# Kernel optimization log

Hardware: AMD Instinct MI355X
Metric: run time of the kernel (lower is better)

Reference implementation:

```python
import jax, jax.numpy as jnp
import numpy as np

N_NODES = 100000
N_EDGES = 3200000
NUM_GRAPHS = 64
NEG_SLOPE = 0.2  # PyG GATConv default leaky_relu slope


def gat_conv(x, src, dst, W, att_src, att_dst, bias, heads, out_ch, concat):
    """PyG GATConv (default args: add_self_loops=True, negative_slope=0.2).
    src/dst already include self loops."""
    n = x.shape[0]
    h = (x @ W).reshape(n, heads, out_ch)              # [N,H,C]
    a_src = jnp.sum(h * att_src, axis=-1)              # [N,H]
    a_dst = jnp.sum(h * att_dst, axis=-1)              # [N,H]
    e = jax.nn.leaky_relu(a_src[src] + a_dst[dst], NEG_SLOPE)  # [E,H]
    # segment softmax over destination nodes
    m = jax.ops.segment_max(e, dst, num_segments=n)
    ex = jnp.exp(e - m[dst])
    denom = jax.ops.segment_sum(ex, dst, num_segments=n)
    alpha = ex / (denom[dst] + 1e-16)                  # [E,H]
    msg = h[src] * alpha[:, :, None]                   # [E,H,C]
    out = jax.ops.segment_sum(msg, dst, num_segments=n)  # [N,H,C]
    if concat:
        out = out.reshape(n, heads * out_ch)
    else:
        out = out.mean(axis=1)
    return out + bias


def setup_inputs() -> dict:
    key = jax.random.key(0)
    ks = jax.random.split(key, 12)
    x = jax.random.normal(ks[0], (N_NODES, 4), dtype=jnp.float32)
    edge_index = jax.random.randint(ks[1], (2, N_EDGES), 0, N_NODES, dtype=jnp.int64)
    batch = jnp.sort(jax.random.randint(ks[2], (N_NODES,), 0, NUM_GRAPHS, dtype=jnp.int64))
    s = 0.1
    return {
        "x": x,
        "edge_index": edge_index,
        "batch": batch,
        "W1": jax.random.normal(ks[3], (4, 64), dtype=jnp.float32) * s,
        "att_src1": jax.random.normal(ks[4], (2, 32), dtype=jnp.float32) * s,
        "att_dst1": jax.random.normal(ks[5], (2, 32), dtype=jnp.float32) * s,
        "bias1": jnp.zeros((64,), dtype=jnp.float32),
        "W2": jax.random.normal(ks[6], (64, 64), dtype=jnp.float32) * s,
        "att_src2": jax.random.normal(ks[7], (1, 64), dtype=jnp.float32) * s,
        "att_dst2": jax.random.normal(ks[8], (1, 64), dtype=jnp.float32) * s,
        "bias2": jnp.zeros((64,), dtype=jnp.float32),
    }


def reference(x, edge_index, batch, W1, att_src1, att_dst1, bias1, W2, att_src2, att_dst2, bias2):
    n = x.shape[0]
    loops = jnp.arange(n, dtype=edge_index.dtype)
    src = jnp.concatenate([edge_index[0], loops])
    dst = jnp.concatenate([edge_index[1], loops])
    h = gat_conv(x, src, dst, W1, att_src1, att_dst1, bias1, heads=2, out_ch=32, concat=True)
    h = jax.nn.elu(h)
    # dropout is identity in eval mode
    h = gat_conv(h, src, dst, W2, att_src2, att_dst2, bias2, heads=1, out_ch=64, concat=False)
    # global_mean_pool
    sums = jax.ops.segment_sum(h, batch, num_segments=NUM_GRAPHS)
    counts = jax.ops.segment_sum(jnp.ones((n,), h.dtype), batch, num_segments=NUM_GRAPHS)
    return sums / jnp.maximum(counts, 1.0)[:, None]
```

## Files before the change

### kernel.cpp

```cpp
#include <hip/hip_runtime.h>
#include <hip/hip_bf16.h>
#include <hip/hip_fp16.h>
#include <math.h>


__device__ __forceinline__ float leaky(float x) { return x >= 0.f ? x : 0.2f * x; }
__device__ __forceinline__ int iclamp(int v, int lo, int hi) {
  return v < lo ? lo : (v > hi ? hi : v);
}
__device__ __forceinline__ unsigned char f8(float v) {
  return (unsigned char)(__builtin_amdgcn_cvt_pk_fp8_f32(v, v, 0, false) & 0xff);
}

typedef __attribute__((ext_vector_type(8))) _Float16 f16x8;
typedef __attribute__((ext_vector_type(4))) float f32x4;
typedef __attribute__((ext_vector_type(2))) float f32x2;

#define NBUCK 1024
#define BSHIFT 7
#define BCAP 4608
#define CSRSZ (NBUCK * BCAP)
#define MAXR 16

__global__ __launch_bounds__(256) void k_att1(
    const float* __restrict__ x, const float* __restrict__ W1,
    const float* __restrict__ att_src1, const float* __restrict__ att_dst1,
    float* __restrict__ a_src1, float* __restrict__ a_dst1, int n) {
  __shared__ float W1s[256];
  int t = threadIdx.x;
  W1s[t] = W1[t];
  __syncthreads();
  int node = blockIdx.x * 4 + (t >> 6);
  int lane = t & 63;
  if (node >= n) return;
  float4 xr = ((const float4*)x)[node];
  float h = xr.x * W1s[lane] + xr.y * W1s[64 + lane] + xr.z * W1s[128 + lane] + xr.w * W1s[192 + lane];
  float vs = h * att_src1[lane];
  float vd = h * att_dst1[lane];
  #pragma unroll
  for (int m = 16; m >= 1; m >>= 1) { vs += __shfl_xor(vs, m); vd += __shfl_xor(vd, m); }
  if ((lane & 31) == 0) {
    int head = lane >> 5;
    a_src1[node * 2 + head] = vs;
    a_dst1[node * 2 + head] = vd;
  }
}

__global__ __launch_bounds__(1024) void k_bscatter(
    const int* __restrict__ ei, int E, int n, int* __restrict__ bcur,
    unsigned* __restrict__ pairs) {
  __shared__ int h[NBUCK];
  __shared__ int cur[NBUCK];
  int t = threadIdx.x;
  if (t < NBUCK) h[t] = 0;
  __syncthreads();
  int chunk = (E + gridDim.x - 1) / gridDim.x;
  int beg = blockIdx.x * chunk;
  int end = beg + chunk; if (end > E) end = E;
  unsigned pR[MAXR];
  unsigned short bR[MAXR];
  int cntr = 0;
  for (int i = beg + t; i < end && cntr < MAXR; i += 1024) {
    int s = iclamp(ei[i], 0, n - 1);
    int d = iclamp(ei[E + i], 0, n - 1);
    int bkt = d >> BSHIFT;
    pR[cntr] = ((unsigned)(d & 127) << 25) | (unsigned)s;
    bR[cntr] = (unsigned short)bkt;
    atomicAdd(&h[bkt], 1);
    ++cntr;
  }
  __syncthreads();
  if (t < NBUCK) cur[t] = t * BCAP + (h[t] ? atomicAdd(&bcur[t], h[t]) : 0);
  __syncthreads();
  for (int k = 0; k < cntr; ++k) {
    int bkt = bR[k];
    int pos = atomicAdd(&cur[bkt], 1);
    if (pos >= bkt * BCAP && pos < (bkt + 1) * BCAP) pairs[pos] = pR[k];
  }
}

__global__ __launch_bounds__(256) void k_bbuild(
    const unsigned* __restrict__ pairs, const int* __restrict__ bcur,
    int n, int* __restrict__ rowbeg, int* __restrict__ rowend,
    int* __restrict__ csr) {
  int b = blockIdx.x;
  int node0 = b << BSHIFT;
  if (node0 >= n) return;
  int base = b * BCAP;
  int cnt = iclamp(bcur[b], 0, BCAP);
  __shared__ int sh[128];
  __shared__ int cur[128];
  int t = threadIdx.x;
  if (t < 128) sh[t] = 0;
  __syncthreads();
  for (int i = t; i < cnt; i += 256)
    atomicAdd(&sh[pairs[base + i] >> 25], 1);
  __syncthreads();
  int v = (t < 128) ? sh[t] : 0;
  for (int ofs = 1; ofs < 128; ofs <<= 1) {
    int u = (t >= ofs && t < 128) ? sh[t - ofs] : 0;
    __syncthreads();
    if (t < 128) sh[t] += u;
    __syncthreads();
  }
  if (t < 128) {
    int off = sh[t] - v;
    cur[t] = off;
    int node = node0 + t;
    if (node < n) {
      rowbeg[node] = base + off;
      rowend[node] = base + off + v;
    }
  }
  __syncthreads();
  for (int i = t; i < cnt; i += 256) {
    unsigned p = pairs[base + i];
    int l = p >> 25;
    int r = atomicAdd(&cur[l], 1);
    int pos = base + r;
    if (pos >= 0 && pos < CSRSZ) csr[pos] = (int)(p & 0x1ffffffu);
  }
}

__global__ __launch_bounds__(256) void k_gat1(
    const float* __restrict__ x, const float* __restrict__ W1,
    const float* __restrict__ a_src1, const float* __restrict__ a_dst1,
    const int* __restrict__ rowbeg, const int* __restrict__ rowend,
    const int* __restrict__ csr,
    const float* __restrict__ bias1, __half* __restrict__ hB,
    int n) {
  __shared__ float W1s[256];
  int t = threadIdx.x;
  W1s[t] = W1[t];
  __syncthreads();
  int lane = t & 63;
  int nd = lane >> 4, sub = lane & 15;
  int node = (blockIdx.x * 4 + (t >> 6)) * 4 + nd;
  bool valid = node < n;
  int nc = valid ? node : 0;
  int beg = valid ? iclamp(rowbeg[nc], 0, CSRSZ) : 0;
  int end = valid ? iclamp(rowend[nc], beg, CSRSZ) : 0;
  float2 ad = ((const float2*)a_dst1)[nc];
  const float4* xp = (const float4*)x;
  const float2* asp = (const float2*)a_src1;
  float A0 = 0.f, A1 = 0.f, A2 = 0.f, A3 = 0.f, dn0 = 0.f;
  float B0 = 0.f, B1 = 0.f, B2 = 0.f, B3 = 0.f, dn1 = 0.f;
  for (int e = beg + sub; e < end; e += 16) {
    int s = iclamp(csr[e], 0, n - 1);
    float2 as = asp[s];
    float ex0 = __expf(leaky(as.x + ad.x));
    float ex1 = __expf(leaky(as.y + ad.y));
    float4 xr = xp[s];
    dn0 += ex0; dn1 += ex1;
    A0 = fmaf(ex0, xr.x, A0); A1 = fmaf(ex0, xr.y, A1);
    A2 = fmaf(ex0, xr.z, A2); A3 = fmaf(ex0, xr.w, A3);
    B0 = fmaf(ex1, xr.x, B0); B1 = fmaf(ex1, xr.y, B1);
    B2 = fmaf(ex1, xr.z, B2); B3 = fmaf(ex1, xr.w, B3);
  }
  bool lo = (sub < 8);
  float C0, C1, C2, C3, dnC, sA, sB;
  sA = __shfl_xor(A0, 8); sB = __shfl_xor(B0, 8); C0 = lo ? A0 + sA : B0 + sB;
  sA = __shfl_xor(A1, 8); sB = __shfl_xor(B1, 8); C1 = lo ? A1 + sA : B1 + sB;
  sA = __shfl_xor(A2, 8); sB = __shfl_xor(B2, 8); C2 = lo ? A2 + sA : B2 + sB;
  sA = __shfl_xor(A3, 8); sB = __shfl_xor(B3, 8); C3 = lo ? A3 + sA : B3 + sB;
  sA = __shfl_xor(dn0, 8); sB = __shfl_xor(dn1, 8); dnC = lo ? dn0 + sA : dn1 + sB;
  #pragma unroll
  for (int m = 4; m >= 1; m >>= 1) {
    C0 += __shfl_xor(C0, m); C1 += __shfl_xor(C1, m);
    C2 += __shfl_xor(C2, m); C3 += __shfl_xor(C3, m);
    dnC += __shfl_xor(dnC, m);
  }
  float2 asn = asp[nc];
  float4 xs = xp[nc];
  float exs = __expf(leaky((lo ? asn.x : asn.y) + (lo ? ad.x : ad.y)));
  dnC += exs;
  C0 = fmaf(exs, xs.x, C0); C1 = fmaf(exs, xs.y, C1);
  C2 = fmaf(exs, xs.z, C2); C3 = fmaf(exs, xs.w, C3);
  float inv = 1.0f / (dnC + 1e-16f);
  if (valid) {
    int f0 = sub * 4;
    float vv[4];
    #pragma unroll
    for (int i = 0; i < 4; ++i) {
      int f = f0 + i;
      float accv = C0 * W1s[f] + C1 * W1s[64 + f] + C2 * W1s[128 + f] + C3 * W1s[192 + f];
      float v = accv * inv + bias1[f];
      vv[i] = v > 0.f ? v : expm1f(v);
    }
    __half2 h01 = __float22half2_rn(make_float2(vv[0], vv[1]));
    __half2 h23 = __float22half2_rn(make_float2(vv[2], vv[3]));
    uint2 pk;
    pk.x = *(unsigned*)&h01;
    pk.y = *(unsigned*)&h23;
    *(uint2*)(hB + (size_t)node * 64 + f0) = pk;
  }
}

__global__ __launch_bounds__(256) void k_lin2(
    const __half* __restrict__ hB, const float* __restrict__ W2,
    const float* __restrict__ att_src2, const float* __restrict__ att_dst2,
    float* __restrict__ a_src2, float* __restrict__ a_dst2,
    unsigned char* __restrict__ hC, int n) {
  __shared__ __attribute__((aligned(16))) _Float16 Whi[64 * 72];
  __shared__ __attribute__((aligned(16))) _Float16 Wlo[64 * 72];
  int t = threadIdx.x;
  for (int i = t; i < 4096; i += 256) {
    int k = i >> 6, col = i & 63;
    float w = W2[i];
    _Float16 hi = (_Float16)w;
    _Float16 lo = (_Float16)(w - (float)hi);
    Whi[col * 72 + k] = hi;
    Wlo[col * 72 + k] = lo;
  }
  __syncthreads();
  int wave = t >> 6, lane = t & 63;
  int quad = lane >> 4, c = lane & 15;
  int m0 = blockIdx.x * 64 + wave * 16;
  if (m0 >= n) return;
  int mrow = m0 + c; if (mrow > n - 1) mrow = n - 1;
  const _Float16* hrow = (const _Float16*)(hB + (size_t)mrow * 64);
  f16x8 a0 = *(const f16x8*)(hrow + quad * 8);
  f16x8 a1 = *(const f16x8*)(hrow + 32 + quad * 8);
  f32x4 zero = {0.f, 0.f, 0.f, 0.f};
  f32x4 acc[4] = {zero, zero, zero, zero};
  #pragma unroll
  for (int tt = 0; tt < 4; ++tt) {
    int nn = tt * 16 + c;
    const _Float16* wh = &Whi[nn * 72];
    const _Float16* wl = &Wlo[nn * 72];
    f16x8 bh0 = *(const f16x8*)(wh + quad * 8);
    f16x8 bh1 = *(const f16x8*)(wh + 32 + quad * 8);
    f16x8 bl0 = *(const f16x8*)(wl + quad * 8);
    f16x8 bl1 = *(const f16x8*)(wl + 32 + quad * 8);
    acc[tt] = __builtin_amdgcn_mfma_f32_16x16x32_f16(a0, bh0, acc[tt], 0, 0, 0);
    acc[tt] = __builtin_amdgcn_mfma_f32_16x16x32_f16(a1, bh1, acc[tt], 0, 0, 0);
    acc[tt] = __builtin_amdgcn_mfma_f32_16x16x32_f16(a0, bl0, acc[tt], 0, 0, 0);
    acc[tt] = __builtin_amdgcn_mfma_f32_16x16x32_f16(a1, bl1, acc[tt], 0, 0, 0);
  }
  float as2[4], ad2[4];
  #pragma unroll
  for (int tt = 0; tt < 4; ++tt) {
    as2[tt] = att_src2[tt * 16 + c];
    ad2[tt] = att_dst2[tt * 16 + c];
  }
  #pragma unroll
  for (int r = 0; r < 4; ++r) {
    float s = 0.f, d = 0.f;
    #pragma unroll
    for (int tt = 0; tt < 4; ++tt) {
      s = fmaf(acc[tt][r], as2[tt], s);
      d = fmaf(acc[tt][r], ad2[tt], d);
    }
    #pragma unroll
    for (int msk = 8; msk >= 1; msk >>= 1) {
      s += __shfl_xor(s, msk);
      d += __shfl_xor(d, msk);
    }
    int m = m0 + quad * 4 + r;
    if (m < n) {
      if (c == 0) { a_src2[m] = s; a_dst2[m] = d; }
      unsigned char* orow = hC + (size_t)m * 64;
      #pragma unroll
      for (int tt = 0; tt < 4; ++tt)
        orow[tt * 16 + c] = f8(acc[tt][r]);
    }
  }
}

__global__ __launch_bounds__(256) void k_gat2(
    const unsigned char* __restrict__ hC, const float* __restrict__ a_src2,
    const float* __restrict__ a_dst2, const int* __restrict__ rowbeg,
    const int* __restrict__ rowend, const int* __restrict__ csr,
    const float* __restrict__ bias2,
    __half* __restrict__ h2, int n) {
  __shared__ unsigned long long stage[4 * 64];
  int t = threadIdx.x;
  int w = t >> 6, lane = t & 63;
  int node = blockIdx.x * 4 + w;
  if (node >= n) return;
  int beg = iclamp(rowbeg[node], 0, CSRSZ);
  int end = iclamp(rowend[node], beg, CSRSZ);
  float ad = a_dst2[node];
  int g = lane >> 3;
  int p = lane & 7;
  const uint2* hrows = (const uint2*)hC;
  unsigned long long* st = &stage[w * 64];
  float ac0 = 0.f, ac1 = 0.f, ac2 = 0.f, ac3 = 0.f;
  float ac4 = 0.f, ac5 = 0.f, ac6 = 0.f, ac7 = 0.f;
  float dn = 0.f;
  for (int tb = beg; tb < end; tb += 64) {
    int tc = end - tb; if (tc > 64) tc = 64;
    int s = 0; float ex = 0.f;
    if (lane < tc) {
      s = iclamp(csr[tb + lane], 0, n - 1);
      ex = __expf(leaky(a_src2[s] + ad));
    }
    dn += ex;
    st[lane] = ((unsigned long long)(unsigned)s << 32) | (unsigned)__float_as_uint(ex);
    int steps = (tc + 7) >> 3;
    int j = 0;
    for (; j + 2 <= steps; j += 2) {
      unsigned long long pk0 = st[j * 8 + g];
      unsigned long long pk1 = st[(j + 1) * 8 + g];
      int s0 = (int)(pk0 >> 32), s1 = (int)(pk1 >> 32);
      float e0 = __uint_as_float((unsigned)pk0);
      float e1 = __uint_as_float((unsigned)pk1);
      uint2 hw0 = hrows[(size_t)s0 * 8 + p];
      uint2 hw1 = hrows[(size_t)s1 * 8 + p];
      f32x2 a, b;
      a = __builtin_amdgcn_cvt_pk_f32_fp8(hw0.x, false);
      b = __builtin_amdgcn_cvt_pk_f32_fp8(hw0.x, true);
      ac0 = fmaf(e0, a.x, ac0); ac1 = fmaf(e0, a.y, ac1);
      ac2 = fmaf(e0, b.x, ac2); ac3 = fmaf(e0, b.y, ac3);
      a = __builtin_amdgcn_cvt_pk_f32_fp8(hw0.y, false);
      b = __builtin_amdgcn_cvt_pk_f32_fp8(hw0.y, true);
      ac4 = fmaf(e0, a.x, ac4); ac5 = fmaf(e0, a.y, ac5);
      ac6 = fmaf(e0, b.x, ac6); ac7 = fmaf(e0, b.y, ac7);
      a = __builtin_amdgcn_cvt_pk_f32_fp8(hw1.x, false);
      b = __builtin_amdgcn_cvt_pk_f32_fp8(hw1.x, true);
      ac0 = fmaf(e1, a.x, ac0); ac1 = fmaf(e1, a.y, ac1);
      ac2 = fmaf(e1, b.x, ac2); ac3 = fmaf(e1, b.y, ac3);
      a = __builtin_amdgcn_cvt_pk_f32_fp8(hw1.y, false);
      b = __builtin_amdgcn_cvt_pk_f32_fp8(hw1.y, true);
      ac4 = fmaf(e1, a.x, ac4); ac5 = fmaf(e1, a.y, ac5);
      ac6 = fmaf(e1, b.x, ac6); ac7 = fmaf(e1, b.y, ac7);
    }
    if (j < steps) {
      unsigned long long pk0 = st[j * 8 + g];
      int s0 = (int)(pk0 >> 32);
      float e0 = __uint_as_float((unsigned)pk0);
      uint2 hw0 = hrows[(size_t)s0 * 8 + p];
      f32x2 a, b;
      a = __builtin_amdgcn_cvt_pk_f32_fp8(hw0.x, false);
      b = __builtin_amdgcn_cvt_pk_f32_fp8(hw0.x, true);
      ac0 = fmaf(e0, a.x, ac0); ac1 = fmaf(e0, a.y, ac1);
      ac2 = fmaf(e0, b.x, ac2); ac3 = fmaf(e0, b.y, ac3);
      a = __builtin_amdgcn_cvt_pk_f32_fp8(hw0.y, false);
      b = __builtin_amdgcn_cvt_pk_f32_fp8(hw0.y, true);
      ac4 = fmaf(e0, a.x, ac4); ac5 = fmaf(e0, a.y, ac5);
      ac6 = fmaf(e0, b.x, ac6); ac7 = fmaf(e0, b.y, ac7);
    }
  }
  #pragma unroll
  for (int m = 8; m <= 32; m <<= 1) {
    ac0 += __shfl_xor(ac0, m); ac1 += __shfl_xor(ac1, m);
    ac2 += __shfl_xor(ac2, m); ac3 += __shfl_xor(ac3, m);
    ac4 += __shfl_xor(ac4, m); ac5 += __shfl_xor(ac5, m);
    ac6 += __shfl_xor(ac6, m); ac7 += __shfl_xor(ac7, m);
  }
  #pragma unroll
  for (int m = 32; m >= 1; m >>= 1) dn += __shfl_xor(dn, m);
  float exs = __expf(leaky(a_src2[node] + ad));
  dn += exs;
  uint2 hs = hrows[(size_t)node * 8 + p];
  {
    f32x2 a, b;
    a = __builtin_amdgcn_cvt_pk_f32_fp8(hs.x, false);
    b = __builtin_amdgcn_cvt_pk_f32_fp8(hs.x, true);
    ac0 = fmaf(exs, a.x, ac0); ac1 = fmaf(exs, a.y, ac1);
    ac2 = fmaf(exs, b.x, ac2); ac3 = fmaf(exs, b.y, ac3);
    a = __builtin_amdgcn_cvt_pk_f32_fp8(hs.y, false);
    b = __builtin_amdgcn_cvt_pk_f32_fp8(hs.y, true);
    ac4 = fmaf(exs, a.x, ac4); ac5 = fmaf(exs, a.y, ac5);
    ac6 = fmaf(exs, b.x, ac6); ac7 = fmaf(exs, b.y, ac7);
  }
  if (g == 0) {
    float inv = 1.0f / (dn + 1e-16f);
    const float* b2 = bias2 + p * 8;
    __half2 o0 = __float22half2_rn(make_float2(ac0 * inv + b2[0], ac1 * inv + b2[1]));
    __half2 o1 = __float22half2_rn(make_float2(ac2 * inv + b2[2], ac3 * inv + b2[3]));
    __half2 o2 = __float22half2_rn(make_float2(ac4 * inv + b2[4], ac5 * inv + b2[5]));
    __half2 o3 = __float22half2_rn(make_float2(ac6 * inv + b2[6], ac7 * inv + b2[7]));
    uint4 pk;
    pk.x = *(unsigned*)&o0; pk.y = *(unsigned*)&o1;
    pk.z = *(unsigned*)&o2; pk.w = *(unsigned*)&o3;
    ((uint4*)(h2 + (size_t)node * 64))[p] = pk;
  }
}

__global__ __launch_bounds__(256) void k_pool(
    const __half* __restrict__ h2, const int* __restrict__ batch,
    float* __restrict__ pool, float* __restrict__ cnt, int n, int G) {
  const int PW = 64;
  int wave = blockIdx.x * 4 + (threadIdx.x >> 6);
  int lane = threadIdx.x & 63;
  int start = wave * PW;
  if (start >= n) return;
  int end = start + PW; if (end > n) end = n;
  int bcur = iclamp(batch[start], 0, G - 1);
  float acc = 0.f, count = 0.f;
  for (int i = start; i < end; ++i) {
    int b = iclamp(batch[i], 0, G - 1);
    if (b != bcur) {
      atomicAdd(&pool[bcur * 64 + lane], acc);
      if (lane == 0) atomicAdd(&cnt[bcur], count);
      bcur = b; acc = 0.f; count = 0.f;
    }
    acc += __half2float(h2[(size_t)i * 64 + lane]);
    count += 1.f;
  }
  atomicAdd(&pool[bcur * 64 + lane], acc);
  if (lane == 0) atomicAdd(&cnt[bcur], count);
}

__global__ void k_final(const float* __restrict__ pool, const float* __restrict__ cnt,
                        float* __restrict__ out, int G) {
  int i = blockIdx.x * blockDim.x + threadIdx.x;
  if (i >= G * 64) return;
  out[i] = pool[i] / fmaxf(cnt[i >> 6], 1.0f);
}

extern "C" void kernel_launch(void* const* d_in, const int* in_sizes, int n_in,
                              void* d_out, int out_size, void* d_ws, size_t ws_size,
                              hipStream_t stream) {
  const float* x        = (const float*)d_in[0];
  const int*   ei       = (const int*)d_in[1];
  const int*   batch    = (const int*)d_in[2];
  const float* W1       = (const float*)d_in[3];
  const float* att_src1 = (const float*)d_in[4];
  const float* att_dst1 = (const float*)d_in[5];
  const float* bias1    = (const float*)d_in[6];
  const float* W2       = (const float*)d_in[7];
  const float* att_src2 = (const float*)d_in[8];
  const float* att_dst2 = (const float*)d_in[9];
  const float* bias2    = (const float*)d_in[10];

  const int n = in_sizes[0] / 4;
  const int E = in_sizes[1] / 2;
  const int G = out_size / 64;

  char* p = (char*)d_ws;
  auto alloc = [&](size_t bytes) -> void* {
    void* r = (void*)p;
    p += (bytes + 255) & ~(size_t)255;
    return r;
  };
  int* csr = (int*)alloc((size_t)CSRSZ * 4);
  size_t hsz = (size_t)n * 64 * 2;
  size_t csz = (size_t)n * 64;
  size_t rsz = hsz + csz;
  if (rsz < (size_t)CSRSZ * 4) rsz = (size_t)CSRSZ * 4;
  char* R = (char*)alloc(rsz);
  unsigned* pairs = (unsigned*)R;
  __half* hB = (__half*)R;
  __half* h2 = (__half*)R;
  unsigned char* hC = (unsigned char*)(R + hsz);
  int*   rowbeg = (int*)alloc((size_t)n * 4);
  int*   rowend = (int*)alloc((size_t)n * 4);
  size_t poolelems = (size_t)G * 64 + G;
  char*  Z = (char*)alloc(poolelems * 4 + (size_t)NBUCK * 4);
  float* pool = (float*)Z;
  float* cnt  = pool + (size_t)G * 64;
  int*   bcur = (int*)(Z + poolelems * 4);
  float* a_src1 = (float*)alloc((size_t)n * 2 * 4);
  float* a_dst1 = (float*)alloc((size_t)n * 2 * 4);
  float* a_src2 = (float*)alloc((size_t)n * 4);
  float* a_dst2 = (float*)alloc((size_t)n * 4);

  hipMemsetAsync(Z, 0, poolelems * 4 + (size_t)NBUCK * 4, stream);

  const int gridN4 = (n + 3) / 4;
  int NBK = (E + MAXR * 1024 - 1) / (MAXR * 1024);
  if (NBK < 256) NBK = 256;

  k_att1<<<gridN4, 256, 0, stream>>>(x, W1, att_src1, att_dst1, a_src1, a_dst1, n);
  k_bscatter<<<NBK, 1024, 0, stream>>>(ei, E, n, bcur, pairs);
  k_bbuild<<<NBUCK, 256, 0, stream>>>(pairs, bcur, n, rowbeg, rowend, csr);
  k_gat1<<<(n + 15) / 16, 256, 0, stream>>>(x, W1, a_src1, a_dst1, rowbeg, rowend, csr, bias1, hB, n);
  k_lin2<<<(n + 63) / 64, 256, 0, stream>>>(hB, W2, att_src2, att_dst2, a_src2, a_dst2, hC, n);
  k_gat2<<<gridN4, 256, 0, stream>>>(hC, a_src2, a_dst2, rowbeg, rowend, csr, bias2, h2, n);
  k_pool<<<(n + 255) / 256, 256, 0, stream>>>(h2, batch, pool, cnt, n, G);
  k_final<<<(G * 64 + 255) / 256, 256, 0, stream>>>(pool, cnt, (float*)d_out, G);
}
```

Measured before the change: 292.9 us.

## Tune bucket scatter occupancy, unroll gat1 edge loop, amortize W2 staging in lin2

Halves the per-thread register batch in the bucket scatter, adds an occupancy hint and raises the minimum block count so more waves are resident. The gat1 edge loop now handles two edges per iteration so more gathers are in flight at once. lin2 has each wave process four 16-row tiles, so the W2 hi/lo conversion into shared memory is paid once per 256 rows instead of once per 64. The cost is fewer lin2 blocks and more registers used in gat1.

```diff
diff --git a/kernel.cpp b/kernel.cpp
--- a/kernel.cpp
+++ b/kernel.cpp
@@ -20,7 +20,7 @@
 #define BSHIFT 7
 #define BCAP 4608
 #define CSRSZ (NBUCK * BCAP)
-#define MAXR 16
+#define MAXR 8
 
 __global__ __launch_bounds__(256) void k_att1(
     const float* __restrict__ x, const float* __restrict__ W1,
@@ -46,7 +46,7 @@
   }
 }
 
-__global__ __launch_bounds__(1024) void k_bscatter(
+__global__ __launch_bounds__(1024, 8) void k_bscatter(
     const int* __restrict__ ei, int E, int n, int* __restrict__ bcur,
     unsigned* __restrict__ pairs) {
   __shared__ int h[NBUCK];
@@ -145,7 +145,29 @@
   const float2* asp = (const float2*)a_src1;
   float A0 = 0.f, A1 = 0.f, A2 = 0.f, A3 = 0.f, dn0 = 0.f;
   float B0 = 0.f, B1 = 0.f, B2 = 0.f, B3 = 0.f, dn1 = 0.f;
-  for (int e = beg + sub; e < end; e += 16) {
+  int e = beg + sub;
+  for (; e + 16 < end; e += 32) {
+    int sa = iclamp(csr[e], 0, n - 1);
+    int sb = iclamp(csr[e + 16], 0, n - 1);
+    float2 asa = asp[sa];
+    float2 asb = asp[sb];
+    float4 xa = xp[sa];
+    float4 xb = xp[sb];
+    float ea0 = __expf(leaky(asa.x + ad.x));
+    float ea1 = __expf(leaky(asa.y + ad.y));
+    float eb0 = __expf(leaky(asb.x + ad.x));
+    float eb1 = __expf(leaky(asb.y + ad.y));
+    dn0 += ea0 + eb0; dn1 += ea1 + eb1;
+    A0 = fmaf(ea0, xa.x, A0); A1 = fmaf(ea0, xa.y, A1);
+    A2 = fmaf(ea0, xa.z, A2); A3 = fmaf(ea0, xa.w, A3);
+    B0 = fmaf(ea1, xa.x, B0); B1 = fmaf(ea1, xa.y, B1);
+    B2 = fmaf(ea1, xa.z, B2); B3 = fmaf(ea1, xa.w, B3);
+    A0 = fmaf(eb0, xb.x, A0); A1 = fmaf(eb0, xb.y, A1);
+    A2 = fmaf(eb0, xb.z, A2); A3 = fmaf(eb0, xb.w, A3);
+    B0 = fmaf(eb1, xb.x, B0); B1 = fmaf(eb1, xb.y, B1);
+    B2 = fmaf(eb1, xb.z, B2); B3 = fmaf(eb1, xb.w, B3);
+  }
+  if (e < end) {
     int s = iclamp(csr[e], 0, n - 1);
     float2 as = asp[s];
     float ex0 = __expf(leaky(as.x + ad.x));
@@ -215,54 +237,56 @@
   __syncthreads();
   int wave = t >> 6, lane = t & 63;
   int quad = lane >> 4, c = lane & 15;
-  int m0 = blockIdx.x * 64 + wave * 16;
-  if (m0 >= n) return;
-  int mrow = m0 + c; if (mrow > n - 1) mrow = n - 1;
-  const _Float16* hrow = (const _Float16*)(hB + (size_t)mrow * 64);
-  f16x8 a0 = *(const f16x8*)(hrow + quad * 8);
-  f16x8 a1 = *(const f16x8*)(hrow + 32 + quad * 8);
-  f32x4 zero = {0.f, 0.f, 0.f, 0.f};
-  f32x4 acc[4] = {zero, zero, zero, zero};
-  #pragma unroll
-  for (int tt = 0; tt < 4; ++tt) {
-    int nn = tt * 16 + c;
-    const _Float16* wh = &Whi[nn * 72];
-    const _Float16* wl = &Wlo[nn * 72];
-    f16x8 bh0 = *(const f16x8*)(wh + quad * 8);
-    f16x8 bh1 = *(const f16x8*)(wh + 32 + quad * 8);
-    f16x8 bl0 = *(const f16x8*)(wl + quad * 8);
-    f16x8 bl1 = *(const f16x8*)(wl + 32 + quad * 8);
-    acc[tt] = __builtin_amdgcn_mfma_f32_16x16x32_f16(a0, bh0, acc[tt], 0, 0, 0);
-    acc[tt] = __builtin_amdgcn_mfma_f32_16x16x32_f16(a1, bh1, acc[tt], 0, 0, 0);
-    acc[tt] = __builtin_amdgcn_mfma_f32_16x16x32_f16(a0, bl0, acc[tt], 0, 0, 0);
-    acc[tt] = __builtin_amdgcn_mfma_f32_16x16x32_f16(a1, bl1, acc[tt], 0, 0, 0);
-  }
   float as2[4], ad2[4];
   #pragma unroll
   for (int tt = 0; tt < 4; ++tt) {
     as2[tt] = att_src2[tt * 16 + c];
     ad2[tt] = att_dst2[tt * 16 + c];
   }
-  #pragma unroll
-  for (int r = 0; r < 4; ++r) {
-    float s = 0.f, d = 0.f;
+  for (int it = 0; it < 4; ++it) {
+    int m0 = blockIdx.x * 256 + wave * 64 + it * 16;
+    if (m0 >= n) break;
+    int mrow = m0 + c; if (mrow > n - 1) mrow = n - 1;
+    const _Float16* hrow = (const _Float16*)(hB + (size_t)mrow * 64);
+    f16x8 a0 = *(const f16x8*)(hrow + quad * 8);
+    f16x8 a1 = *(const f16x8*)(hrow + 32 + quad * 8);
+    f32x4 zero = {0.f, 0.f, 0.f, 0.f};
+    f32x4 acc[4] = {zero, zero, zero, zero};
     #pragma unroll
     for (int tt = 0; tt < 4; ++tt) {
-      s = fmaf(acc[tt][r], as2[tt], s);
-      d = fmaf(acc[tt][r], ad2[tt], d);
+      int nn = tt * 16 + c;
+      const _Float16* wh = &Whi[nn * 72];
+      const _Float16* wl = &Wlo[nn * 72];
+      f16x8 bh0 = *(const f16x8*)(wh + quad * 8);
+      f16x8 bh1 = *(const f16x8*)(wh + 32 + quad * 8);
+      f16x8 bl0 = *(const f16x8*)(wl + quad * 8);
+      f16x8 bl1 = *(const f16x8*)(wl + 32 + quad * 8);
+      acc[tt] = __builtin_amdgcn_mfma_f32_16x16x32_f16(a0, bh0, acc[tt], 0, 0, 0);
+      acc[tt] = __builtin_amdgcn_mfma_f32_16x16x32_f16(a1, bh1, acc[tt], 0, 0, 0);
+      acc[tt] = __builtin_amdgcn_mfma_f32_16x16x32_f16(a0, bl0, acc[tt], 0, 0, 0);
+      acc[tt] = __builtin_amdgcn_mfma_f32_16x16x32_f16(a1, bl1, acc[tt], 0, 0, 0);
     }
     #pragma unroll
-    for (int msk = 8; msk >= 1; msk >>= 1) {
-      s += __shfl_xor(s, msk);
-      d += __shfl_xor(d, msk);
-    }
-    int m = m0 + quad * 4 + r;
-    if (m < n) {
-      if (c == 0) { a_src2[m] = s; a_dst2[m] = d; }
-      unsigned char* orow = hC + (size_t)m * 64;
+    for (int r = 0; r < 4; ++r) {
+      float s = 0.f, d = 0.f;
       #pragma unroll
-      for (int tt = 0; tt < 4; ++tt)
-        orow[tt * 16 + c] = f8(acc[tt][r]);
+      for (int tt = 0; tt < 4; ++tt) {
+        s = fmaf(acc[tt][r], as2[tt], s);
+        d = fmaf(acc[tt][r], ad2[tt], d);
+      }
+      #pragma unroll
+      for (int msk = 8; msk >= 1; msk >>= 1) {
+        s += __shfl_xor(s, msk);
+        d += __shfl_xor(d, msk);
+      }
+      int m = m0 + quad * 4 + r;
+      if (m < n) {
+        if (c == 0) { a_src2[m] = s; a_dst2[m] = d; }
+        unsigned char* orow = hC + (size_t)m * 64;
+        #pragma unroll
+        for (int tt = 0; tt < 4; ++tt)
+          orow[tt * 16 + c] = f8(acc[tt][r]);
+      }
     }
   }
 }
@@ -461,13 +485,13 @@
 
   const int gridN4 = (n + 3) / 4;
   int NBK = (E + MAXR * 1024 - 1) / (MAXR * 1024);
-  if (NBK < 256) NBK = 256;
+  if (NBK < 512) NBK = 512;
 
   k_att1<<<gridN4, 256, 0, stream>>>(x, W1, att_src1, att_dst1, a_src1, a_dst1, n);
   k_bscatter<<<NBK, 1024, 0, stream>>>(ei, E, n, bcur, pairs);
   k_bbuild<<<NBUCK, 256, 0, stream>>>(pairs, bcur, n, rowbeg, rowend, csr);
   k_gat1<<<(n + 15) / 16, 256, 0, stream>>>(x, W1, a_src1, a_dst1, rowbeg, rowend, csr, bias1, hB, n);
-  k_lin2<<<(n + 63) / 64, 256, 0, stream>>>(hB, W2, att_src2, att_dst2, a_src2, a_dst2, hC, n);
+  k_lin2<<<(n + 255) / 256, 256, 0, stream>>>(hB, W2, att_src2, att_dst2, a_src2, a_dst2, hC, n);
   k_gat2<<<gridN4, 256, 0, stream>>>(hC, a_src2, a_dst2, rowbeg, rowend, csr, bias2, h2, n);
   k_pool<<<(n + 255) / 256, 256, 0, stream>>>(h2, batch, pool, cnt, n, G);
   k_final<<<(G * 64 + 255) / 256, 256, 0, stream>>>(pool, cnt, (float*)d_out, G);
```

Result: no change. 292.4 us (-0.2%).
